# Kernel tuning notes

Measured on AMD Instinct MI355X. Metric: run time of the kernel, lower is better.

Reference implementation:

```python
import jax, jax.numpy as jnp
import numpy as np

NUM_HEADS = 8
NUM_POINTS = 4
NUM_PIP = 4  # num_points_in_pillar
RADIUS = 0.12


def grid_sample_bilinear(feat, grid):
    """torch.nn.functional.grid_sample(mode='bilinear', padding_mode='zeros', align_corners=False).
    feat: [G, D, H, W], grid: [G, Q, P, 2] in [-1, 1] (x=width, y=height) -> [G, Q, P, D]."""
    G, D, H, W = feat.shape
    Q, P = grid.shape[1], grid.shape[2]
    x = (grid[..., 0] + 1.0) * 0.5 * W - 0.5
    y = (grid[..., 1] + 1.0) * 0.5 * H - 0.5
    x0 = jnp.floor(x)
    y0 = jnp.floor(y)
    feat_flat = feat.reshape(G, D, H * W).transpose(0, 2, 1)  # [G, HW, D]
    out = jnp.zeros((G, Q * P, D), dtype=feat.dtype)
    for dx, dy in ((0, 0), (1, 0), (0, 1), (1, 1)):
        xi = x0 + dx
        yi = y0 + dy
        w = (1.0 - jnp.abs(x - xi)) * (1.0 - jnp.abs(y - yi))
        valid = (xi >= 0) & (xi <= W - 1) & (yi >= 0) & (yi <= H - 1)
        xi_c = jnp.clip(xi, 0, W - 1).astype(jnp.int32)
        yi_c = jnp.clip(yi, 0, H - 1).astype(jnp.int32)
        idx = (yi_c * W + xi_c).reshape(G, Q * P)
        g = jnp.take_along_axis(feat_flat, idx[:, :, None], axis=1)  # [G, Q*P, D]
        out = out + g * (w * valid.astype(w.dtype)).reshape(G, Q * P, 1)
    return out.reshape(G, Q, P, D)


def setup_inputs() -> dict:
    key = jax.random.key(0)
    ks = jax.random.split(key, 8)
    B, N, C = 1, 2500, 256
    cams, H, W = 6, 46, 80
    return {
        "query": jax.random.normal(ks[0], (B, N, C), dtype=jnp.float32),
        "image_feats": jax.random.normal(ks[1], (B, cams, C, H, W), dtype=jnp.float32),
        "reference_points_cam": jax.random.uniform(ks[2], (B, cams, N, NUM_PIP, 2), dtype=jnp.float32),
        "bev_mask": jax.random.uniform(ks[3], (B, cams, N, NUM_PIP)) > 0.3,
        "offset_w": jax.random.normal(ks[4], (NUM_HEADS * NUM_PIP * NUM_POINTS * 2, C), dtype=jnp.float32) * 0.02,
        "offset_b": jnp.zeros((NUM_HEADS * NUM_PIP * NUM_POINTS * 2,), dtype=jnp.float32),
        "weight_w": jax.random.normal(ks[5], (NUM_HEADS * NUM_PIP * NUM_POINTS, C), dtype=jnp.float32) * 0.02,
        "weight_b": jnp.zeros((NUM_HEADS * NUM_PIP * NUM_POINTS,), dtype=jnp.float32),
        "out_w": jax.random.normal(ks[6], (C, C), dtype=jnp.float32) * 0.02,
        "out_b": jnp.zeros((C,), dtype=jnp.float32),
    }


def reference(query, image_feats, reference_points_cam, bev_mask,
              offset_w, offset_b, weight_w, weight_b, out_w, out_b):
    B, N, C = query.shape
    cams, H, W = image_feats.shape[1], image_feats.shape[3], image_feats.shape[4]
    heads, PiP, P = NUM_HEADS, NUM_PIP, NUM_POINTS
    K = PiP * P
    D = C // heads

    # Per-query learned offsets and attention logits
    offsets = jnp.tanh(query @ offset_w.T + offset_b).reshape(B, N, heads, PiP, P, 2) * RADIUS
    wl = (query @ weight_w.T + weight_b).reshape(B, N, heads, K)  # [B,N,h,K]

    # Sampling locations per camera: ref [B,cams,N,PiP,2] + offsets -> [B,cams,N,h,K,2]
    loc = reference_points_cam[:, :, :, None, :, None, :] + offsets[:, None]
    loc = loc.reshape(B, cams, N, heads, K, 2)

    # Visibility mask broadcast to points: [B,cams,N,h,K]
    vis = jnp.broadcast_to(bev_mask[:, :, :, None, :, None], (B, cams, N, heads, PiP, P))
    vis = vis.reshape(B, cams, N, heads, K)

    # Masked softmax over K (handles fully-masked rows)
    m = vis.astype(wl.dtype)
    logits = jnp.where(vis, wl[:, None], jnp.asarray(-1e9, wl.dtype))
    w = jax.nn.softmax(logits, axis=-1) * m
    w = w / jnp.clip(jnp.sum(w, axis=-1, keepdims=True), 1e-6)

    # grid_sample over all (batch, cam, head) at once
    grid = loc.transpose(0, 1, 3, 2, 4, 5).reshape(B * cams * heads, N, K, 2) * 2.0 - 1.0
    feat = image_feats.reshape(B * cams * heads, D, H, W)
    sampled = grid_sample_bilinear(feat, grid)  # [B*cams*h, N, K, D]
    sampled = sampled.reshape(B, cams, heads, N, K, D).transpose(0, 1, 3, 2, 4, 5)  # [B,cams,N,h,K,D]

    cam_out = jnp.sum(sampled * w[..., None], axis=4).reshape(B, cams, N, C)

    has_vis = jnp.any(bev_mask, axis=-1)  # [B,cams,N]
    cam_out = cam_out * has_vis[..., None].astype(cam_out.dtype)

    fused = jnp.sum(cam_out, axis=1)  # [B,N,C]
    counts = jnp.clip(jnp.sum(has_vis.astype(jnp.int32), axis=1), 1)  # [B,N]
    fused = fused / counts[..., None].astype(fused.dtype)
    return fused @ out_w.T + out_b
```

## Files before the change

kernel.cpp:

```cpp
#include <hip/hip_runtime.h>
#include <math.h>

#define CAMS 6
#define CCH 256
#define HH 46
#define WW 80
#define NPIX (HH * WW)
#define HEADS 8
#define PIP 4
#define PP 4
#define KK 16
#define RADIUS_F 0.12f

__device__ __forceinline__ unsigned short f2bf(float f) {
    unsigned int x = __float_as_uint(f);
    unsigned int r = (x + 0x7FFFu + ((x >> 16) & 1u)) >> 16;
    return (unsigned short)r;
}
__device__ __forceinline__ float bf2f(unsigned short u) {
    return __uint_as_float(((unsigned int)u) << 16);
}

__global__ void __launch_bounds__(256) feat_transpose_k(const float* __restrict__ in,
                                                        unsigned short* __restrict__ out) {
    __shared__ float tile[64][65];
    int cam = blockIdx.z;
    int r0 = blockIdx.y * 64;
    int p0 = blockIdx.x * 64;
    int tj = threadIdx.x & 63;
    int ti = threadIdx.x >> 6;
    const float* src = in + ((long)cam * CCH + r0) * NPIX + p0;
#pragma unroll
    for (int k = 0; k < 64; k += 4) {
        if (p0 + tj < NPIX) tile[ti + k][tj] = src[(long)(ti + k) * NPIX + tj];
    }
    __syncthreads();
    unsigned short* dst = out + ((long)cam * NPIX + p0) * CCH + r0;
#pragma unroll
    for (int k = 0; k < 64; k += 4) {
        if (p0 + ti + k < NPIX) dst[(long)(ti + k) * CCH + tj] = f2bf(tile[tj][ti + k]);
    }
}

__global__ void __launch_bounds__(256) wtrans_k(const float* __restrict__ offw,
                                                const float* __restrict__ ww,
                                                const float* __restrict__ outw,
                                                float* __restrict__ offT,
                                                float* __restrict__ wT,
                                                float* __restrict__ outT) {
    __shared__ float tile[64][65];
    int b = blockIdx.x;
    const float* src;
    float* dst;
    int R, C, tr, tc;
    if (b < 16)      { src = offw; dst = offT; R = 256; C = 256; tr = b >> 2;        tc = b & 3; }
    else if (b < 24) { src = ww;   dst = wT;   R = 128; C = 256; tr = (b - 16) >> 2; tc = (b - 16) & 3; }
    else             { src = outw; dst = outT; R = 256; C = 256; tr = (b - 24) >> 2; tc = (b - 24) & 3; }
    int tj = threadIdx.x & 63;
    int ti = threadIdx.x >> 6;
#pragma unroll
    for (int k = 0; k < 64; k += 4)
        tile[ti + k][tj] = src[(long)(tr * 64 + ti + k) * C + tc * 64 + tj];
    __syncthreads();
#pragma unroll
    for (int k = 0; k < 64; k += 4)
        dst[(long)(tc * 64 + ti + k) * R + tr * 64 + tj] = tile[tj][ti + k];
}

template <int NT>
__global__ void qgemm_k(const float* __restrict__ query,
                        const float* __restrict__ offT,
                        const float* __restrict__ offB,
                        const float* __restrict__ wT,
                        const float* __restrict__ wB,
                        float* __restrict__ offsets,
                        float* __restrict__ wl,
                        int N) {
    __shared__ float q[NT][CCH];
    int n0 = blockIdx.x * NT;
    int tid = threadIdx.x;
    for (int t = 0; t < NT; t++) {
        int n = n0 + t;
        q[t][tid] = (n < N) ? query[(long)n * CCH + tid] : 0.f;
    }
    __syncthreads();

    {
        float acc[NT];
        float b = offB[tid];
#pragma unroll
        for (int t = 0; t < NT; t++) acc[t] = b;
        for (int j = 0; j < CCH; j++) {
            float wv = offT[j * CCH + tid];
#pragma unroll
            for (int t = 0; t < NT; t++) acc[t] = fmaf(q[t][j], wv, acc[t]);
        }
        for (int t = 0; t < NT; t++) {
            int n = n0 + t;
            if (n < N) offsets[(long)n * CCH + tid] = tanhf(acc[t]) * RADIUS_F;
        }
    }
    if (tid < 128) {
        float acc[NT];
        float b = wB[tid];
#pragma unroll
        for (int t = 0; t < NT; t++) acc[t] = b;
        for (int j = 0; j < CCH; j++) {
            float wv = wT[j * 128 + tid];
#pragma unroll
            for (int t = 0; t < NT; t++) acc[t] = fmaf(q[t][j], wv, acc[t]);
        }
        for (int t = 0; t < NT; t++) {
            int n = n0 + t;
            if (n < N) wl[(long)n * 128 + tid] = acc[t];
        }
    }
}

__global__ void __launch_bounds__(256, 4) sample_cam_k(
        const unsigned short* __restrict__ feat_t,
        const float* __restrict__ refp,
        const int* __restrict__ bev,
        const float* __restrict__ offsets,
        const float* __restrict__ wl,
        float* __restrict__ cam_out,
        int N, int per_xcd) {
    int xcd = blockIdx.x & 7;
    int local = (blockIdx.x >> 3) * 4 + (threadIdx.x >> 6);
    if (local >= per_xcd) return;
    long task = (long)xcd * per_xcd + local;
    if (task >= (long)CAMS * N) return;
    int cam = (int)(task / N);
    int n = (int)(task - (long)cam * N);

    int l = threadIdx.x & 63;
    int h = l >> 3;

    const int* bv = bev + ((long)cam * N + n) * 4;
    int m0 = bv[0], m1 = bv[1], m2 = bv[2], m3 = bv[3];
    float* outp = cam_out + ((long)cam * N + n) * CCH + (l << 2);
    if (!(m0 | m1 | m2 | m3)) {
        *(float4*)outp = make_float4(0.f, 0.f, 0.f, 0.f);
        return;
    }

    const float* rp = refp + ((long)cam * N + n) * 8;
    const float4* offn = (const float4*)(offsets + (long)n * CCH + (h << 5));
    const float4* wln = (const float4*)(wl + (long)n * 128 + (h << 4));

    float4 wl0, wl1, wl2, wl3;
    float mmax = -1e30f;
    if (m0) { wl0 = wln[0]; mmax = fmaxf(mmax, fmaxf(fmaxf(wl0.x, wl0.y), fmaxf(wl0.z, wl0.w))); }
    if (m1) { wl1 = wln[1]; mmax = fmaxf(mmax, fmaxf(fmaxf(wl1.x, wl1.y), fmaxf(wl1.z, wl1.w))); }
    if (m2) { wl2 = wln[2]; mmax = fmaxf(mmax, fmaxf(fmaxf(wl2.x, wl2.y), fmaxf(wl2.z, wl2.w))); }
    if (m3) { wl3 = wln[3]; mmax = fmaxf(mmax, fmaxf(fmaxf(wl3.x, wl3.y), fmaxf(wl3.z, wl3.w))); }

    float w_[KK];
#pragma unroll
    for (int k = 0; k < KK; k++) w_[k] = 0.f;
    float ssum = 0.f;
    if (m0) {
        w_[0] = __expf(wl0.x - mmax); w_[1] = __expf(wl0.y - mmax);
        w_[2] = __expf(wl0.z - mmax); w_[3] = __expf(wl0.w - mmax);
        ssum += w_[0] + w_[1] + w_[2] + w_[3];
    }
    if (m1) {
        w_[4] = __expf(wl1.x - mmax); w_[5] = __expf(wl1.y - mmax);
        w_[6] = __expf(wl1.z - mmax); w_[7] = __expf(wl1.w - mmax);
        ssum += w_[4] + w_[5] + w_[6] + w_[7];
    }
    if (m2) {
        w_[8] = __expf(wl2.x - mmax); w_[9] = __expf(wl2.y - mmax);
        w_[10] = __expf(wl2.z - mmax); w_[11] = __expf(wl2.w - mmax);
        ssum += w_[8] + w_[9] + w_[10] + w_[11];
    }
    if (m3) {
        w_[12] = __expf(wl3.x - mmax); w_[13] = __expf(wl3.y - mmax);
        w_[14] = __expf(wl3.z - mmax); w_[15] = __expf(wl3.w - mmax);
        ssum += w_[12] + w_[13] + w_[14] + w_[15];
    }
    float inv = 1.f / ssum;

    const ushort4* fcam = (const ushort4*)(feat_t + (long)cam * NPIX * CCH) + l;
    float ax = 0.f, ay = 0.f, az = 0.f, aw = 0.f;

#pragma unroll
    for (int pip = 0; pip < PIP; pip++) {
        int vis = (pip == 0) ? m0 : (pip == 1) ? m1 : (pip == 2) ? m2 : m3;
        if (!vis) continue;
        float rx = rp[pip * 2 + 0];
        float ry = rp[pip * 2 + 1];
        float4 oa = offn[pip * 2];
        float4 ob = offn[pip * 2 + 1];
        float px[PP] = {oa.x, oa.z, ob.x, ob.z};
        float py[PP] = {oa.y, oa.w, ob.y, ob.w};
#pragma unroll
        for (int p = 0; p < PP; p++) {
            float wgt = w_[pip * PP + p];
            float x = fmaf(rx + px[p], (float)WW, -0.5f);
            float y = fmaf(ry + py[p], (float)HH, -0.5f);
            float x0f = floorf(x), y0f = floorf(y);
            float fx = x - x0f, fy = y - y0f;
            int ix = (int)x0f, iy = (int)y0f;
            int ix0 = min(max(ix, 0), WW - 1);
            int ix1 = min(max(ix + 1, 0), WW - 1);
            int iy0 = min(max(iy, 0), HH - 1);
            int iy1 = min(max(iy + 1, 0), HH - 1);
            float wx0 = (1.f - fx) * (((ix >= 0) & (ix < WW)) ? 1.f : 0.f);
            float wx1 = fx * (((ix + 1 >= 0) & (ix + 1 < WW)) ? 1.f : 0.f);
            float wy0 = (1.f - fy) * (((iy >= 0) & (iy < HH)) ? 1.f : 0.f);
            float wy1 = fy * (((iy + 1 >= 0) & (iy + 1 < HH)) ? 1.f : 0.f);
            const ushort4 u00 = fcam[(iy0 * WW + ix0) * (CCH / 4)];
            const ushort4 u01 = fcam[(iy0 * WW + ix1) * (CCH / 4)];
            const ushort4 u10 = fcam[(iy1 * WW + ix0) * (CCH / 4)];
            const ushort4 u11 = fcam[(iy1 * WW + ix1) * (CCH / 4)];
            float a00 = wgt * wy0 * wx0;
            float a01 = wgt * wy0 * wx1;
            float a10 = wgt * wy1 * wx0;
            float a11 = wgt * wy1 * wx1;
            ax = fmaf(a00, bf2f(u00.x), ax); ay = fmaf(a00, bf2f(u00.y), ay);
            az = fmaf(a00, bf2f(u00.z), az); aw = fmaf(a00, bf2f(u00.w), aw);
            ax = fmaf(a01, bf2f(u01.x), ax); ay = fmaf(a01, bf2f(u01.y), ay);
            az = fmaf(a01, bf2f(u01.z), az); aw = fmaf(a01, bf2f(u01.w), aw);
            ax = fmaf(a10, bf2f(u10.x), ax); ay = fmaf(a10, bf2f(u10.y), ay);
            az = fmaf(a10, bf2f(u10.z), az); aw = fmaf(a10, bf2f(u10.w), aw);
            ax = fmaf(a11, bf2f(u11.x), ax); ay = fmaf(a11, bf2f(u11.y), ay);
            az = fmaf(a11, bf2f(u11.z), az); aw = fmaf(a11, bf2f(u11.w), aw);
        }
    }
    *(float4*)outp = make_float4(ax * inv, ay * inv, az * inv, aw * inv);
}

template <int NT>
__global__ void outproj_fuse_k(const float* __restrict__ cam_out,
                               const int* __restrict__ bev,
                               const float* __restrict__ outT,
                               const float* __restrict__ outB,
                               float* __restrict__ out, int N) {
    __shared__ float f[NT][CCH];
    __shared__ float inv_s[NT];
    int n0 = blockIdx.x * NT;
    int tid = threadIdx.x;
    for (int t = 0; t < NT; t++) {
        int n = n0 + t;
        float sum = 0.f;
        if (n < N) {
#pragma unroll
            for (int cam = 0; cam < CAMS; cam++)
                sum += cam_out[((long)cam * N + n) * CCH + tid];
        }
        f[t][tid] = sum;
    }
    if (tid < NT) {
        int n = n0 + tid;
        int cnt = 0;
        if (n < N) {
#pragma unroll
            for (int cam = 0; cam < CAMS; cam++) {
                const int* bv = bev + ((long)cam * N + n) * 4;
                cnt += (bv[0] | bv[1] | bv[2] | bv[3]) ? 1 : 0;
            }
        }
        inv_s[tid] = 1.f / (float)max(cnt, 1);
    }
    __syncthreads();
    float acc[NT];
#pragma unroll
    for (int t = 0; t < NT; t++) acc[t] = 0.f;
    for (int j = 0; j < CCH; j++) {
        float wv = outT[j * CCH + tid];
#pragma unroll
        for (int t = 0; t < NT; t++) acc[t] = fmaf(f[t][j], wv, acc[t]);
    }
    float b = outB[tid];
    for (int t = 0; t < NT; t++) {
        int n = n0 + t;
        if (n < N) out[(long)n * CCH + tid] = fmaf(acc[t], inv_s[t], b);
    }
}

extern "C" void kernel_launch(void* const* d_in, const int* in_sizes, int n_in,
                              void* d_out, int out_size, void* d_ws, size_t ws_size,
                              hipStream_t stream) {
    const float* query    = (const float*)d_in[0];
    const float* imfeat   = (const float*)d_in[1];
    const float* refp     = (const float*)d_in[2];
    const int*   bev      = (const int*)d_in[3];
    const float* offset_w = (const float*)d_in[4];
    const float* offset_b = (const float*)d_in[5];
    const float* weight_w = (const float*)d_in[6];
    const float* weight_b = (const float*)d_in[7];
    const float* out_w    = (const float*)d_in[8];
    const float* out_b    = (const float*)d_in[9];
    float* out = (float*)d_out;

    int N = in_sizes[0] / CCH;

    float* ws = (float*)d_ws;
    unsigned short* feat_t = (unsigned short*)ws;
    float* offT   = ws + (size_t)CAMS * NPIX * CCH / 2;
    float* wTw    = offT + (size_t)CCH * CCH;
    float* outT   = wTw + (size_t)128 * CCH;
    float* offs   = outT + (size_t)CCH * CCH;
    float* wl     = offs + (size_t)N * CCH;
    float* camob  = wl + (size_t)N * 128;

    feat_transpose_k<<<dim3((NPIX + 63) / 64, CCH / 64, CAMS), 256, 0, stream>>>(imfeat, feat_t);
    wtrans_k<<<40, 256, 0, stream>>>(offset_w, weight_w, out_w, offT, wTw, outT);

    qgemm_k<8><<<(N + 7) / 8, 256, 0, stream>>>(query, offT, offset_b, wTw, weight_b,
                                                offs, wl, N);

    int T = CAMS * N;
    int per_xcd = (T + 7) / 8;
    int blocks = 8 * ((per_xcd + 3) / 4);
    sample_cam_k<<<blocks, 256, 0, stream>>>(feat_t, refp, bev, offs, wl, camob,
                                             N, per_xcd);

    outproj_fuse_k<8><<<(N + 7) / 8, 256, 0, stream>>>(camob, bev, outT, out_b, out, N);
}
```

Before: 111.5 us.

## Remap query and output projections to one wavefront per query

Both small GEMM kernels now assign one wavefront to each query row, with each lane computing several output columns, instead of a block computing one column for eight queries. The offset and attention-weight matrices are concatenated into a single 256x384 transposed matrix, so one fused pass produces both outputs. The intent is more blocks and fewer block barriers. The cost is that weights are no longer reused across queries within a block, so every wave re-reads the whole weight matrix and relies on cache hits.

```diff
diff --git a/kernel.cpp b/kernel.cpp
--- a/kernel.cpp
+++ b/kernel.cpp
@@ -11,6 +11,7 @@
 #define PP 4
 #define KK 16
 #define RADIUS_F 0.12f
+#define NC 384
 
 __device__ __forceinline__ unsigned short f2bf(float f) {
     unsigned int x = __float_as_uint(f);
@@ -45,17 +46,17 @@
 __global__ void __launch_bounds__(256) wtrans_k(const float* __restrict__ offw,
                                                 const float* __restrict__ ww,
                                                 const float* __restrict__ outw,
-                                                float* __restrict__ offT,
-                                                float* __restrict__ wT,
+                                                float* __restrict__ WC,
                                                 float* __restrict__ outT) {
     __shared__ float tile[64][65];
     int b = blockIdx.x;
     const float* src;
     float* dst;
-    int R, C, tr, tc;
-    if (b < 16)      { src = offw; dst = offT; R = 256; C = 256; tr = b >> 2;        tc = b & 3; }
-    else if (b < 24) { src = ww;   dst = wT;   R = 128; C = 256; tr = (b - 16) >> 2; tc = (b - 16) & 3; }
-    else             { src = outw; dst = outT; R = 256; C = 256; tr = (b - 24) >> 2; tc = (b - 24) & 3; }
+    int C, tr, tc, dstride, dcol0;
+    if (b < 16)      { src = offw; dst = WC;   C = 256; tr = b >> 2;        tc = b & 3;        dstride = NC;  dcol0 = 0; }
+    else if (b < 24) { src = ww;   dst = WC;   C = 256; tr = (b - 16) >> 2; tc = (b - 16) & 3; dstride = NC;  dcol0 = 256; }
+    else             { src = outw; dst = outT; C = 256; tr = (b - 24) >> 2; tc = (b - 24) & 3; dstride = 256; dcol0 = 0; }
+    if (b >= 16 && b < 24) { tr = (b - 16) & 1; tc = (b - 16) >> 1; }
     int tj = threadIdx.x & 63;
     int ti = threadIdx.x >> 6;
 #pragma unroll
@@ -64,56 +65,44 @@
     __syncthreads();
 #pragma unroll
     for (int k = 0; k < 64; k += 4)
-        dst[(long)(tc * 64 + ti + k) * R + tr * 64 + tj] = tile[tj][ti + k];
-}
-
-template <int NT>
-__global__ void qgemm_k(const float* __restrict__ query,
-                        const float* __restrict__ offT,
-                        const float* __restrict__ offB,
-                        const float* __restrict__ wT,
-                        const float* __restrict__ wB,
-                        float* __restrict__ offsets,
-                        float* __restrict__ wl,
-                        int N) {
-    __shared__ float q[NT][CCH];
-    int n0 = blockIdx.x * NT;
-    int tid = threadIdx.x;
-    for (int t = 0; t < NT; t++) {
-        int n = n0 + t;
-        q[t][tid] = (n < N) ? query[(long)n * CCH + tid] : 0.f;
-    }
-    __syncthreads();
-
-    {
-        float acc[NT];
-        float b = offB[tid];
-#pragma unroll
-        for (int t = 0; t < NT; t++) acc[t] = b;
-        for (int j = 0; j < CCH; j++) {
-            float wv = offT[j * CCH + tid];
-#pragma unroll
-            for (int t = 0; t < NT; t++) acc[t] = fmaf(q[t][j], wv, acc[t]);
-        }
-        for (int t = 0; t < NT; t++) {
-            int n = n0 + t;
-            if (n < N) offsets[(long)n * CCH + tid] = tanhf(acc[t]) * RADIUS_F;
-        }
-    }
-    if (tid < 128) {
-        float acc[NT];
-        float b = wB[tid];
-#pragma unroll
-        for (int t = 0; t < NT; t++) acc[t] = b;
-        for (int j = 0; j < CCH; j++) {
-            float wv = wT[j * 128 + tid];
-#pragma unroll
-            for (int t = 0; t < NT; t++) acc[t] = fmaf(q[t][j], wv, acc[t]);
-        }
-        for (int t = 0; t < NT; t++) {
-            int n = n0 + t;
-            if (n < N) wl[(long)n * 128 + tid] = acc[t];
-        }
+        dst[(long)(tc * 64 + ti + k) * dstride + dcol0 + tr * 64 + tj] = tile[tj][ti + k];
+}
+
+__global__ void __launch_bounds__(256) qgemm2_k(const float* __restrict__ query,
+                                                const float* __restrict__ WC,
+                                                const float* __restrict__ offB,
+                                                const float* __restrict__ wB,
+                                                float* __restrict__ offsets,
+                                                float* __restrict__ wl,
+                                                int N) {
+    __shared__ float qs[4][CCH];
+    int w = threadIdx.x >> 6, l = threadIdx.x & 63;
+    int n = blockIdx.x * 4 + w;
+    if (n >= N) return;
+    const float* qr = query + (long)n * CCH;
+    qs[w][l] = qr[l];
+    qs[w][l + 64] = qr[l + 64];
+    qs[w][l + 128] = qr[l + 128];
+    qs[w][l + 192] = qr[l + 192];
+
+    float acc[6] = {0.f, 0.f, 0.f, 0.f, 0.f, 0.f};
+    const float* wp = WC + l;
+#pragma unroll 4
+    for (int j = 0; j < CCH; j++) {
+        float qj = qs[w][j];
+        const float* row = wp + (long)j * NC;
+#pragma unroll
+        for (int i = 0; i < 6; i++) acc[i] = fmaf(qj, row[i * 64], acc[i]);
+    }
+#pragma unroll
+    for (int i = 0; i < 4; i++) {
+        int col = l + 64 * i;
+        offsets[(long)n * CCH + col] = tanhf(acc[i] + offB[col]) * RADIUS_F;
+    }
+#pragma unroll
+    for (int i = 4; i < 6; i++) {
+        int col = l + 64 * (i - 4);
+        wl[(long)n * 128 + col] = acc[i] + wB[col];
     }
 }
 
@@ -231,51 +220,46 @@
     *(float4*)outp = make_float4(ax * inv, ay * inv, az * inv, aw * inv);
 }
 
-template <int NT>
-__global__ void outproj_fuse_k(const float* __restrict__ cam_out,
-                               const int* __restrict__ bev,
-                               const float* __restrict__ outT,
-                               const float* __restrict__ outB,
-                               float* __restrict__ out, int N) {
-    __shared__ float f[NT][CCH];
-    __shared__ float inv_s[NT];
-    int n0 = blockIdx.x * NT;
-    int tid = threadIdx.x;
-    for (int t = 0; t < NT; t++) {
-        int n = n0 + t;
+__global__ void __launch_bounds__(256) outproj2_k(const float* __restrict__ cam_out,
+                                                  const int* __restrict__ bev,
+                                                  const float* __restrict__ outT,
+                                                  const float* __restrict__ outB,
+                                                  float* __restrict__ out, int N) {
+    __shared__ float fs[4][CCH];
+    int w = threadIdx.x >> 6, l = threadIdx.x & 63;
+    int n = blockIdx.x * 4 + w;
+    if (n >= N) return;
+
+#pragma unroll
+    for (int i = 0; i < 4; i++) {
+        int ch = l + 64 * i;
         float sum = 0.f;
-        if (n < N) {
-#pragma unroll
-            for (int cam = 0; cam < CAMS; cam++)
-                sum += cam_out[((long)cam * N + n) * CCH + tid];
-        }
-        f[t][tid] = sum;
-    }
-    if (tid < NT) {
-        int n = n0 + tid;
-        int cnt = 0;
-        if (n < N) {
-#pragma unroll
-            for (int cam = 0; cam < CAMS; cam++) {
-                const int* bv = bev + ((long)cam * N + n) * 4;
-                cnt += (bv[0] | bv[1] | bv[2] | bv[3]) ? 1 : 0;
-            }
-        }
-        inv_s[tid] = 1.f / (float)max(cnt, 1);
-    }
-    __syncthreads();
-    float acc[NT];
-#pragma unroll
-    for (int t = 0; t < NT; t++) acc[t] = 0.f;
+#pragma unroll
+        for (int cam = 0; cam < CAMS; cam++)
+            sum += cam_out[((long)cam * N + n) * CCH + ch];
+        fs[w][ch] = sum;
+    }
+    int cnt = 0;
+#pragma unroll
+    for (int cam = 0; cam < CAMS; cam++) {
+        const int* bv = bev + ((long)cam * N + n) * 4;
+        cnt += (bv[0] | bv[1] | bv[2] | bv[3]) ? 1 : 0;
+    }
+    float inv = 1.f / (float)max(cnt, 1);
+
+    float acc[4] = {0.f, 0.f, 0.f, 0.f};
+    const float* wp = outT + l;
+#pragma unroll 4
     for (int j = 0; j < CCH; j++) {
-        float wv = outT[j * CCH + tid];
-#pragma unroll
-        for (int t = 0; t < NT; t++) acc[t] = fmaf(f[t][j], wv, acc[t]);
-    }
-    float b = outB[tid];
-    for (int t = 0; t < NT; t++) {
-        int n = n0 + t;
-        if (n < N) out[(long)n * CCH + tid] = fmaf(acc[t], inv_s[t], b);
+        float fj = fs[w][j];
+        const float* row = wp + (long)j * CCH;
+#pragma unroll
+        for (int i = 0; i < 4; i++) acc[i] = fmaf(fj, row[i * 64], acc[i]);
+    }
+#pragma unroll
+    for (int i = 0; i < 4; i++) {
+        int col = l + 64 * i;
+        out[(long)n * CCH + col] = fmaf(acc[i], inv, outB[col]);
     }
 }
 
@@ -298,18 +282,16 @@
 
     float* ws = (float*)d_ws;
     unsigned short* feat_t = (unsigned short*)ws;
-    float* offT   = ws + (size_t)CAMS * NPIX * CCH / 2;
-    float* wTw    = offT + (size_t)CCH * CCH;
-    float* outT   = wTw + (size_t)128 * CCH;
+    float* WC     = ws + (size_t)CAMS * NPIX * CCH / 2;
+    float* outT   = WC + (size_t)CCH * NC;
     float* offs   = outT + (size_t)CCH * CCH;
     float* wl     = offs + (size_t)N * CCH;
     float* camob  = wl + (size_t)N * 128;
 
     feat_transpose_k<<<dim3((NPIX + 63) / 64, CCH / 64, CAMS), 256, 0, stream>>>(imfeat, feat_t);
-    wtrans_k<<<40, 256, 0, stream>>>(offset_w, weight_w, out_w, offT, wTw, outT);
-
-    qgemm_k<8><<<(N + 7) / 8, 256, 0, stream>>>(query, offT, offset_b, wTw, weight_b,
-                                                offs, wl, N);
+    wtrans_k<<<40, 256, 0, stream>>>(offset_w, weight_w, out_w, WC, outT);
+
+    qgemm2_k<<<(N + 3) / 4, 256, 0, stream>>>(query, WC, offset_b, weight_b, offs, wl, N);
 
     int T = CAMS * N;
     int per_xcd = (T + 7) / 8;
@@ -317,5 +299,5 @@
     sample_cam_k<<<blocks, 256, 0, stream>>>(feat_t, refp, bev, offs, wl, camob,
                                              N, per_xcd);
 
-    outproj_fuse_k<8><<<(N + 7) / 8, 256, 0, stream>>>(camob, bev, outT, out_b, out, N);
-}
+    outproj2_k<<<(N + 3) / 4, 256, 0, stream>>>(camob, bev, outT, out_b, out, N);
+}
```

New measurement: 111.7 us. No clear change (+0.2%).
